# Kernel tuning notes

Measured on AMD Instinct MI355X. Metric: run time of the kernel, lower is better.

## Reference

```python
import jax, jax.numpy as jnp
import numpy as np

N, E, DIM, H = 50000, 800000, 256, 4
HD = DIM // H  # per-head dim = 64
NEG_SLOPE = 0.2
EPS = 1e-5


def _layernorm(x, g, b):
    mu = jnp.mean(x, axis=-1, keepdims=True)
    var = jnp.mean(jnp.square(x - mu), axis=-1, keepdims=True)
    return (x - mu) * jax.lax.rsqrt(var + EPS) * g + b


def setup_inputs() -> dict:
    key = jax.random.key(0)
    ks = jax.random.split(key, 8)
    s = 1.0 / np.sqrt(DIM)
    return {
        "x": jax.random.normal(ks[0], (N, DIM), dtype=jnp.float32),
        "edge_index": jax.random.randint(ks[1], (2, E), 0, N, dtype=jnp.int64),
        "W": jax.random.normal(ks[2], (DIM, DIM), dtype=jnp.float32) * s,
        "a_src": jax.random.normal(ks[3], (H, HD), dtype=jnp.float32) * s,
        "a_dst": jax.random.normal(ks[4], (H, HD), dtype=jnp.float32) * s,
        "gat_b": jnp.zeros((DIM,), jnp.float32),
        "ln1_g": jnp.ones((DIM,), jnp.float32),
        "ln1_b": jnp.zeros((DIM,), jnp.float32),
        "W1": jax.random.normal(ks[5], (DIM, 2 * DIM), dtype=jnp.float32) * s,
        "b1": jnp.zeros((2 * DIM,), jnp.float32),
        "W2": jax.random.normal(ks[6], (2 * DIM, DIM), dtype=jnp.float32) * (1.0 / np.sqrt(2 * DIM)),
        "b2": jnp.zeros((DIM,), jnp.float32),
        "ln2_g": jnp.ones((DIM,), jnp.float32),
        "ln2_b": jnp.zeros((DIM,), jnp.float32),
    }


def _gat(x, edge_index, W, a_src, a_dst, gat_b):
    # add self-loops (PyG GATConv default)
    loops = jnp.arange(N, dtype=edge_index.dtype)
    src = jnp.concatenate([edge_index[0], loops])
    dst = jnp.concatenate([edge_index[1], loops])
    h = (x @ W).reshape(N, H, HD)                    # [N,H,D]
    al_src = jnp.einsum("nhd,hd->nh", h, a_src)      # [N,H]
    al_dst = jnp.einsum("nhd,hd->nh", h, a_dst)
    e = jax.nn.leaky_relu(al_src[src] + al_dst[dst], NEG_SLOPE)  # [E',H]
    # softmax over edges grouped by destination node
    emax = jax.ops.segment_max(e, dst, num_segments=N)           # [N,H]
    ex = jnp.exp(e - emax[dst])
    denom = jax.ops.segment_sum(ex, dst, num_segments=N)         # [N,H]
    alpha = ex / denom[dst]                                      # [E',H]
    msg = alpha[:, :, None] * h[src]                             # [E',H,D]
    out = jax.ops.segment_sum(msg, dst, num_segments=N)          # [N,H,D]
    return out.reshape(N, DIM) + gat_b


def reference(x, edge_index, W, a_src, a_dst, gat_b, ln1_g, ln1_b, W1, b1, W2, b2, ln2_g, ln2_b):
    res = x
    y = _gat(x, edge_index, W, a_src, a_dst, gat_b)
    y = _layernorm(y + res, ln1_g, ln1_b)
    res = y
    f = jax.nn.gelu(y @ W1 + b1, approximate=False) @ W2 + b2
    return _layernorm(f + res, ln2_g, ln2_b)
```

## Files before the change

kernel.cpp:

```cpp
#include <hip/hip_runtime.h>

typedef __bf16 bf16_t;
typedef __bf16 bf16x4 __attribute__((ext_vector_type(4)));
typedef __bf16 bf16x8 __attribute__((ext_vector_type(8)));
typedef float  f32x4  __attribute__((ext_vector_type(4)));
typedef unsigned u32x2 __attribute__((ext_vector_type(2)));

__device__ inline float loadf(const void* p, size_t i, int bf) {
    return bf ? (float)((const bf16_t*)p)[i] : ((const float*)p)[i];
}
__device__ inline int eidx(const void* p, size_t i, int i64) {
    return i64 ? (int)((const long long*)p)[i] : ((const int*)p)[i];
}
__device__ inline float bflo(unsigned u) { return __uint_as_float(u << 16); }
__device__ inline float bfhi(unsigned u) { return __uint_as_float(u & 0xFFFF0000u); }

__device__ inline void gload16(const bf16_t* g, char* l) {
    __builtin_amdgcn_global_load_lds(
        (const __attribute__((address_space(1))) unsigned*)g,
        (__attribute__((address_space(3))) unsigned*)l, 16, 0, 0);
}

__global__ void detect_k(const void* __restrict__ x, const void* __restrict__ ei,
                         int E, int* __restrict__ flags) {
    int l = threadIdx.x;
    const unsigned* xu = (const unsigned*)x;
    unsigned low = xu[l] & 0xFFFFu;
    unsigned ex = (low >> 7) & 0xFF;
    int cnt = __popcll(__ballot(ex >= 115 && ex <= 133));
    const unsigned* eu = (const unsigned*)ei;
    int lim = E < 64 ? E : 64;
    unsigned v = (l < lim) ? eu[2 * (size_t)l + 1] : 0u;
    unsigned long long nz = __ballot(v != 0u);
    if (l == 0) { flags[0] = (cnt >= 32) ? 1 : 0; flags[1] = (nz == 0ull) ? 1 : 0; }
}

__global__ void tobf16_k(const void* __restrict__ in, bf16_t* __restrict__ out,
                         long n, const int* __restrict__ flags) {
    int bf = flags[0];
    long i = ((long)blockIdx.x * 256 + threadIdx.x) * 8;
    long stride = (long)gridDim.x * 256 * 8;
    if (bf) {
        for (; i < n; i += stride)
            *(bf16x8*)&out[i] = *(const bf16x8*)((const bf16_t*)in + i);
    } else {
        for (; i < n; i += stride) {
            f32x4 a = *(const f32x4*)((const float*)in + i);
            f32x4 b = *(const f32x4*)((const float*)in + i + 4);
            bf16x8 r;
            r[0]=(bf16_t)a[0]; r[1]=(bf16_t)a[1]; r[2]=(bf16_t)a[2]; r[3]=(bf16_t)a[3];
            r[4]=(bf16_t)b[0]; r[5]=(bf16_t)b[1]; r[6]=(bf16_t)b[2]; r[7]=(bf16_t)b[3];
            *(bf16x8*)&out[i] = r;
        }
    }
}

__global__ void transpose_k(const void* __restrict__ in, bf16_t* __restrict__ out,
                            int R, int C, const int* __restrict__ flags) {
    int bf = flags[0];
    int i = blockIdx.x * 256 + threadIdx.x;
    if (i < R * C) { int r = i / C, c = i % C; out[c * R + r] = (bf16_t)loadf(in, i, bf); }
}

__global__ __launch_bounds__(256) void gemm128(const bf16_t* __restrict__ A,
                                               const bf16_t* __restrict__ BT,
                                               const void* __restrict__ bias,
                                               bf16_t* __restrict__ C,
                                               int M, int N, int K, int act,
                                               const int* __restrict__ flags,
                                               const void* __restrict__ a_srcp,
                                               const void* __restrict__ a_dstp,
                                               float* __restrict__ alsrc,
                                               float* __restrict__ aldst, int do_al) {
    int bf = flags[0];
    __shared__ __align__(16) char smem[34816];
    int t = threadIdx.x;
    int tm = blockIdx.x * 128;
    int tn = blockIdx.y * 128;
    int w = t >> 6, l = t & 63;
    int wr = (w >> 1) * 64, wc = (w & 1) * 64;
    int lr16 = l & 15, kg = l >> 4;
    int NK = K >> 5;

    f32x4 acc[4][4];
#pragma unroll
    for (int i = 0; i < 4; i++)
#pragma unroll
        for (int j = 0; j < 4; j++) acc[i][j] = (f32x4){0.f, 0.f, 0.f, 0.f};

    bool fast = (tm + 128 <= M);

    if (fast) {
        int buf = 0;
#pragma unroll
        for (int ii = 0; ii < 2; ii++) {
            int c = w + ii * 4;
            int rowa = tm + (c & 1) * 64 + l;
            int rowb = tn + (c & 1) * 64 + l;
            int kc = (c >> 1) * 8;
            gload16(A  + (size_t)rowa * K + kc, smem +         c * 1024 + l * 16);
            gload16(BT + (size_t)rowb * K + kc, smem + 16384 + c * 1024 + l * 16);
        }
        __syncthreads();
        for (int ks = 0; ks < NK; ks++) {
            if (ks + 1 < NK) {
                int k0 = (ks + 1) << 5;
                char* ab = smem + (buf ^ 1) * 8192;
                char* bb = smem + 16384 + (buf ^ 1) * 8192;
#pragma unroll
                for (int ii = 0; ii < 2; ii++) {
                    int c = w + ii * 4;
                    int rowa = tm + (c & 1) * 64 + l;
                    int rowb = tn + (c & 1) * 64 + l;
                    int kc = k0 + (c >> 1) * 8;
                    gload16(A  + (size_t)rowa * K + kc, ab + c * 1024 + l * 16);
                    gload16(BT + (size_t)rowb * K + kc, bb + c * 1024 + l * 16);
                }
            }
            const char* ab = smem + buf * 8192;
            const char* bb = smem + 16384 + buf * 8192;
            bf16x8 af[4], bg[4];
#pragma unroll
            for (int i = 0; i < 4; i++) {
                af[i] = *(const bf16x8*)(ab + ((size_t)(kg * 128 + wr + i * 16 + lr16)) * 16);
                bg[i] = *(const bf16x8*)(bb + ((size_t)(kg * 128 + wc + i * 16 + lr16)) * 16);
            }
#pragma unroll
            for (int i = 0; i < 4; i++)
#pragma unroll
                for (int j = 0; j < 4; j++)
                    acc[i][j] = __builtin_amdgcn_mfma_f32_16x16x32_bf16(af[i], bg[j], acc[i][j], 0, 0, 0);
            __syncthreads();
            buf ^= 1;
        }
    } else {
        int r = t >> 2, kg2 = t & 3;
        for (int ks = 0; ks < NK; ks++) {
            int k0 = ks << 5;
            bf16x8 va[2], vb[2];
#pragma unroll
            for (int j = 0; j < 2; j++) {
                int row = r + j * 64;
                int ra = tm + row; if (ra > M - 1) ra = M - 1;
                va[j] = *(const bf16x8*)(A + (size_t)ra * K + k0 + kg2 * 8);
                vb[j] = *(const bf16x8*)(BT + (size_t)(tn + row) * K + k0 + kg2 * 8);
            }
            __syncthreads();
#pragma unroll
            for (int j = 0; j < 2; j++) {
                int row = r + j * 64;
                *(bf16x8*)(smem + ((size_t)(kg2 * 128 + row)) * 16) = va[j];
                *(bf16x8*)(smem + 16384 + ((size_t)(kg2 * 128 + row)) * 16) = vb[j];
            }
            __syncthreads();
            bf16x8 af[4], bg[4];
#pragma unroll
            for (int i = 0; i < 4; i++) {
                af[i] = *(const bf16x8*)(smem + ((size_t)(kg * 128 + wr + i * 16 + lr16)) * 16);
                bg[i] = *(const bf16x8*)(smem + 16384 + ((size_t)(kg * 128 + wc + i * 16 + lr16)) * 16);
            }
#pragma unroll
            for (int i = 0; i < 4; i++)
#pragma unroll
                for (int j = 0; j < 4; j++)
                    acc[i][j] = __builtin_amdgcn_mfma_f32_16x16x32_bf16(af[i], bg[j], acc[i][j], 0, 0, 0);
        }
        __syncthreads();
    }

    int cr0 = kg * 4;

    if (do_al) {
        float asv[4], adv[4];
#pragma unroll
        for (int j = 0; j < 4; j++) {
            int col = tn + wc + j * 16 + lr16;
            asv[j] = loadf(a_srcp, col, bf);
            adv[j] = loadf(a_dstp, col, bf);
        }
        int head = (tn + wc) >> 6;
#pragma unroll
        for (int i = 0; i < 4; i++) {
#pragma unroll
            for (int q = 0; q < 4; q++) {
                float ps = acc[i][0][q]*asv[0] + acc[i][1][q]*asv[1] + acc[i][2][q]*asv[2] + acc[i][3][q]*asv[3];
                float pd = acc[i][0][q]*adv[0] + acc[i][1][q]*adv[1] + acc[i][2][q]*adv[2] + acc[i][3][q]*adv[3];
#pragma unroll
                for (int d = 1; d < 16; d <<= 1) { ps += __shfl_xor(ps, d); pd += __shfl_xor(pd, d); }
                int row = tm + wr + i * 16 + cr0 + q;
                if (lr16 == 0 && row < M) { alsrc[row * 4 + head] = ps; aldst[row * 4 + head] = pd; }
            }
        }
    }

    bf16_t (*Cst)[136] = (bf16_t(*)[136])smem;
#pragma unroll
    for (int i = 0; i < 4; i++) {
#pragma unroll
        for (int j = 0; j < 4; j++) {
            int col = wc + j * 16 + lr16;
            float bv = bias ? loadf(bias, tn + col, bf) : 0.f;
#pragma unroll
            for (int q = 0; q < 4; q++) {
                float v = acc[i][j][q] + bv;
                if (act) v = 0.5f * v * (1.f + erff(v * 0.70710678118f));
                Cst[wr + i * 16 + cr0 + q][col] = (bf16_t)v;
            }
        }
    }
    __syncthreads();
#pragma unroll
    for (int it = 0; it < 8; it++) {
        int idx = it * 256 + t;
        int row = idx >> 4;
        int c8 = (idx & 15) * 8;
        if (tm + row < M)
            *(bf16x8*)&C[(size_t)(tm + row) * N + tn + c8] = *(const bf16x8*)&Cst[row][c8];
    }
}

__global__ void deg_k(const void* __restrict__ ei, int* __restrict__ deg, int E, int N,
                      const int* __restrict__ flags) {
    int i64 = flags[1];
    int i = blockIdx.x * 256 + threadIdx.x;
    if (i < E) {
        int d = eidx(ei, (size_t)E + i, i64);
        if ((unsigned)d >= (unsigned)N) d = 0;
        atomicAdd(&deg[d], 1);
    }
}

__global__ __launch_bounds__(256) void scan1(const int* __restrict__ deg, int* __restrict__ offs,
                                             int* __restrict__ chunkSum) {
    __shared__ int s[256];
    int t = threadIdx.x, b = blockIdx.x;
    int v = deg[b * 256 + t];
    s[t] = v; __syncthreads();
#pragma unroll
    for (int d = 1; d < 256; d <<= 1) {
        int u = (t >= d) ? s[t - d] : 0;
        __syncthreads(); s[t] += u; __syncthreads();
    }
    offs[b * 256 + t] = s[t] - v;
    if (t == 255) chunkSum[b] = s[255];
}

__global__ __launch_bounds__(256) void scan2(const int* __restrict__ chunkSum, int* __restrict__ chunkOff, int nch) {
    __shared__ int s[256];
    int t = threadIdx.x;
    int v = (t < nch) ? chunkSum[t] : 0;
    s[t] = v; __syncthreads();
#pragma unroll
    for (int d = 1; d < 256; d <<= 1) {
        int u = (t >= d) ? s[t - d] : 0;
        __syncthreads(); s[t] += u; __syncthreads();
    }
    chunkOff[t] = s[t] - v;
}

__global__ void scan3(int* __restrict__ offs, const int* __restrict__ chunkOff,
                      int* __restrict__ cursor, int total) {
    int i = blockIdx.x * 256 + threadIdx.x;
    if (i < total) { int v = offs[i] + chunkOff[i >> 8]; offs[i] = v; cursor[i] = v; }
}

__global__ void scatter_k(const void* __restrict__ ei, int* __restrict__ cursor,
                          int* __restrict__ csr, bf16_t* __restrict__ ewsb,
                          const float* __restrict__ alsrc, const float* __restrict__ aldst,
                          int E, int N, const int* __restrict__ flags) {
    int i64 = flags[1];
    int i = blockIdx.x * 256 + threadIdx.x;
    if (i < E) {
        int s = eidx(ei, i, i64);
        int d = eidx(ei, (size_t)E + i, i64);
        if ((unsigned)s >= (unsigned)N) s = 0;
        if ((unsigned)d >= (unsigned)N) d = 0;
        int p = atomicAdd(&cursor[d], 1);
        csr[p] = s;
        f32x4 as4 = *(const f32x4*)&alsrc[s * 4];
        f32x4 ad4 = *(const f32x4*)&aldst[d * 4];
        bf16x4 w4;
#pragma unroll
        for (int hh = 0; hh < 4; hh++) {
            float e = as4[hh] + ad4[hh];
            e = e > 0.f ? e : 0.2f * e;
            w4[hh] = (bf16_t)expf(fminf(e, 30.f));
        }
        *(bf16x4*)&ewsb[4 * (size_t)p] = w4;
    }
}

__global__ __launch_bounds__(256) void gat_agg_ln(
    const bf16_t* __restrict__ hbuf, const bf16_t* __restrict__ xb,
    const float* __restrict__ alsrc, const float* __restrict__ aldst,
    const int* __restrict__ offs, const int* __restrict__ csr,
    const bf16_t* __restrict__ ewsb,
    const void* __restrict__ gatb, const void* __restrict__ lng, const void* __restrict__ lnb,
    bf16_t* __restrict__ y, const int* __restrict__ flags, int N) {
    int bf = flags[0];
    int w = threadIdx.x >> 6, l = threadIdx.x & 63;
    int n = blockIdx.x * 4 + w;
    if (n >= N) return;
    int h = l >> 4;
    int col0 = l * 4;

    __shared__ int   srcs[4][64];
    __shared__ float ewt[4][4][68];

    int off = offs[n], deg = offs[n + 1] - off;

    float es = alsrc[n * 4 + h] + aldst[n * 4 + h];
    es = es > 0.f ? es : 0.2f * es;
    float wself = expf(fminf(es, 30.f));

    float a0 = 0.f, a1 = 0.f, a2 = 0.f, a3 = 0.f;
    f32x4 ssum = (f32x4){0.f, 0.f, 0.f, 0.f};

    for (int c0 = 0; c0 < deg; c0 += 64) {
        int cl = deg - c0; if (cl > 64) cl = 64;
        if (l < cl) {
            int sv = csr[off + c0 + l];
            srcs[w][l] = sv;
            bf16x4 wv4 = *(const bf16x4*)&ewsb[4 * (size_t)(off + c0 + l)];
            float w0 = (float)wv4[0], w1 = (float)wv4[1], w2 = (float)wv4[2], w3 = (float)wv4[3];
            ewt[w][0][l] = w0; ewt[w][1][l] = w1;
            ewt[w][2][l] = w2; ewt[w][3][l] = w3;
            ssum += (f32x4){w0, w1, w2, w3};
        }
        int i = 0;
        for (; i + 8 <= cl; i += 8) {
            int sv[8]; u32x2 vv[8];
#pragma unroll
            for (int k = 0; k < 8; k++) sv[k] = __builtin_amdgcn_readfirstlane(srcs[w][i + k]);
#pragma unroll
            for (int k = 0; k < 8; k++) vv[k] = ((const u32x2*)(hbuf + (size_t)sv[k] * 256))[l];
            f32x4 wqa = *(const f32x4*)&ewt[w][h][i];
            f32x4 wqb = *(const f32x4*)&ewt[w][h][i + 4];
#pragma unroll
            for (int k = 0; k < 4; k++) {
                a0 += wqa[k]*bflo(vv[k][0]); a1 += wqa[k]*bfhi(vv[k][0]);
                a2 += wqa[k]*bflo(vv[k][1]); a3 += wqa[k]*bfhi(vv[k][1]);
                a0 += wqb[k]*bflo(vv[k+4][0]); a1 += wqb[k]*bfhi(vv[k+4][0]);
                a2 += wqb[k]*bflo(vv[k+4][1]); a3 += wqb[k]*bfhi(vv[k+4][1]);
            }
        }
        for (; i + 4 <= cl; i += 4) {
            int s0 = __builtin_amdgcn_readfirstlane(srcs[w][i]);
            int s1 = __builtin_amdgcn_readfirstlane(srcs[w][i + 1]);
            int s2 = __builtin_amdgcn_readfirstlane(srcs[w][i + 2]);
            int s3 = __builtin_amdgcn_readfirstlane(srcs[w][i + 3]);
            u32x2 v0 = ((const u32x2*)(hbuf + (size_t)s0 * 256))[l];
            u32x2 v1 = ((const u32x2*)(hbuf + (size_t)s1 * 256))[l];
            u32x2 v2 = ((const u32x2*)(hbuf + (size_t)s2 * 256))[l];
            u32x2 v3 = ((const u32x2*)(hbuf + (size_t)s3 * 256))[l];
            f32x4 wq = *(const f32x4*)&ewt[w][h][i];
            a0 += wq[0]*bflo(v0[0]); a1 += wq[0]*bfhi(v0[0]); a2 += wq[0]*bflo(v0[1]); a3 += wq[0]*bfhi(v0[1]);
            a0 += wq[1]*bflo(v1[0]); a1 += wq[1]*bfhi(v1[0]); a2 += wq[1]*bflo(v1[1]); a3 += wq[1]*bfhi(v1[1]);
            a0 += wq[2]*bflo(v2[0]); a1 += wq[2]*bfhi(v2[0]); a2 += wq[2]*bflo(v2[1]); a3 += wq[2]*bfhi(v2[1]);
            a0 += wq[3]*bflo(v3[0]); a1 += wq[3]*bfhi(v3[0]); a2 += wq[3]*bflo(v3[1]); a3 += wq[3]*bfhi(v3[1]);
        }
        for (; i < cl; i++) {
            int sv = __builtin_amdgcn_readfirstlane(srcs[w][i]);
            float wgt = ewt[w][h][i];
            u32x2 v0 = ((const u32x2*)(hbuf + (size_t)sv * 256))[l];
            a0 += wgt*bflo(v0[0]); a1 += wgt*bfhi(v0[0]); a2 += wgt*bflo(v0[1]); a3 += wgt*bfhi(v0[1]);
        }
    }

#pragma unroll
    for (int d = 1; d < 64; d <<= 1) {
        ssum[0] += __shfl_xor(ssum[0], d);
        ssum[1] += __shfl_xor(ssum[1], d);
        ssum[2] += __shfl_xor(ssum[2], d);
        ssum[3] += __shfl_xor(ssum[3], d);
    }
    float dsum = (h == 0) ? ssum[0] : (h == 1) ? ssum[1] : (h == 2) ? ssum[2] : ssum[3];
    float di = 1.f / (dsum + wself);

    u32x2 sv2 = ((const u32x2*)(hbuf + (size_t)n * 256))[l];
    u32x2 xv  = ((const u32x2*)(xb   + (size_t)n * 256))[l];
    float v0f = (a0 + wself*bflo(sv2[0])) * di + loadf(gatb, col0 + 0, bf) + bflo(xv[0]);
    float v1f = (a1 + wself*bfhi(sv2[0])) * di + loadf(gatb, col0 + 1, bf) + bfhi(xv[0]);
    float v2f = (a2 + wself*bflo(sv2[1])) * di + loadf(gatb, col0 + 2, bf) + bflo(xv[1]);
    float v3f = (a3 + wself*bfhi(sv2[1])) * di + loadf(gatb, col0 + 3, bf) + bfhi(xv[1]);

    float s1 = v0f + v1f + v2f + v3f;
#pragma unroll
    for (int d = 1; d < 64; d <<= 1) s1 += __shfl_xor(s1, d);
    float mu = s1 * (1.f / 256.f);
    float c0f = v0f - mu, c1f = v1f - mu, c2f = v2f - mu, c3f = v3f - mu;
    float sq = c0f*c0f + c1f*c1f + c2f*c2f + c3f*c3f;
#pragma unroll
    for (int d = 1; d < 64; d <<= 1) sq += __shfl_xor(sq, d);
    float rs = rsqrtf(sq * (1.f / 256.f) + 1e-5f);

    bf16x4 o;
    o[0] = (bf16_t)(c0f * rs * loadf(lng, col0 + 0, bf) + loadf(lnb, col0 + 0, bf));
    o[1] = (bf16_t)(c1f * rs * loadf(lng, col0 + 1, bf) + loadf(lnb, col0 + 1, bf));
    o[2] = (bf16_t)(c2f * rs * loadf(lng, col0 + 2, bf) + loadf(lnb, col0 + 2, bf));
    o[3] = (bf16_t)(c3f * rs * loadf(lng, col0 + 3, bf) + loadf(lnb, col0 + 3, bf));
    *(bf16x4*)&y[(size_t)n * 256 + col0] = o;
}

__global__ __launch_bounds__(256) void ln_res(const bf16_t* __restrict__ f, const bf16_t* __restrict__ y,
                                              const void* __restrict__ g, const void* __restrict__ b,
                                              void* __restrict__ out, int N, const int* __restrict__ flags) {
    int bf = flags[0];
    int row = blockIdx.x * 4 + (threadIdx.x >> 6);
    int l = threadIdx.x & 63;
    if (row >= N) return;
    int col0 = l * 4;
    u32x2 fv = *(const u32x2*)(f + (size_t)row * 256 + col0);
    u32x2 yv = *(const u32x2*)(y + (size_t)row * 256 + col0);
    float v0 = bflo(fv[0]) + bflo(yv[0]);
    float v1 = bfhi(fv[0]) + bfhi(yv[0]);
    float v2 = bflo(fv[1]) + bflo(yv[1]);
    float v3 = bfhi(fv[1]) + bfhi(yv[1]);
    float s = v0 + v1 + v2 + v3;
#pragma unroll
    for (int d = 1; d < 64; d <<= 1) s += __shfl_xor(s, d);
    float mu = s * (1.f / 256.f);
    float c0 = v0 - mu, c1 = v1 - mu, c2 = v2 - mu, c3 = v3 - mu;
    float sq = c0*c0 + c1*c1 + c2*c2 + c3*c3;
#pragma unroll
    for (int d = 1; d < 64; d <<= 1) sq += __shfl_xor(sq, d);
    float rs = rsqrtf(sq * (1.f / 256.f) + 1e-5f);
    float o0 = c0 * rs * loadf(g, col0 + 0, bf) + loadf(b, col0 + 0, bf);
    float o1 = c1 * rs * loadf(g, col0 + 1, bf) + loadf(b, col0 + 1, bf);
    float o2 = c2 * rs * loadf(g, col0 + 2, bf) + loadf(b, col0 + 2, bf);
    float o3 = c3 * rs * loadf(g, col0 + 3, bf) + loadf(b, col0 + 3, bf);
    if (bf) {
        bf16x4 o; o[0]=(bf16_t)o0; o[1]=(bf16_t)o1; o[2]=(bf16_t)o2; o[3]=(bf16_t)o3;
        *(bf16x4*)&((bf16_t*)out)[(size_t)row * 256 + col0] = o;
    } else {
        f32x4 o = (f32x4){o0, o1, o2, o3};
        *(f32x4*)&((float*)out)[(size_t)row * 256 + col0] = o;
    }
}

extern "C" void kernel_launch(void* const* d_in, const int* in_sizes, int n_in,
                              void* d_out, int out_size, void* d_ws, size_t ws_size,
                              hipStream_t stream) {
    const void* x    = d_in[0];
    const void* ei   = d_in[1];
    const void* W    = d_in[2];
    const void* a_src= d_in[3];
    const void* a_dst= d_in[4];
    const void* gatb = d_in[5];
    const void* ln1g = d_in[6];
    const void* ln1b = d_in[7];
    const void* W1   = d_in[8];
    const void* b1   = d_in[9];
    const void* W2   = d_in[10];
    const void* b2   = d_in[11];
    const void* ln2g = d_in[12];
    const void* ln2b = d_in[13];

    const int DIM = 256, DFF = 512;
    int N = in_sizes[0] / DIM;
    int E = in_sizes[1] / 2;

    char* ws = (char*)d_ws;
    size_t o = 0;
    auto alloc = [&](size_t bytes) { void* p = ws + o; o += (bytes + 255) & ~(size_t)255; return p; };
    int*    flags  = (int*)alloc(256);
    bf16_t* WT     = (bf16_t*)alloc((size_t)DIM * DIM * 2);
    bf16_t* W1T    = (bf16_t*)alloc((size_t)DIM * DFF * 2);
    bf16_t* W2T    = (bf16_t*)alloc((size_t)DFF * DIM * 2);
    float*  alsrc  = (float*)alloc((size_t)N * 4 * 4);
    float*  aldst  = (float*)alloc((size_t)N * 4 * 4);
    int nch = (N + 255) / 256;
    int tot = nch * 256;
    int* deg      = (int*)alloc((size_t)tot * 4);
    int* offs     = (int*)alloc((size_t)(tot + 1) * 4);
    int* cursor   = (int*)alloc((size_t)tot * 4);
    int* chunkSum = (int*)alloc(256 * 4);
    int* chunkOff = (int*)alloc(256 * 4);
    int* csr      = (int*)alloc((size_t)E * 4);
    bf16_t* ewsb  = (bf16_t*)alloc((size_t)E * 8);
    bf16_t* h     = (bf16_t*)alloc((size_t)N * DIM * 2);
    bf16_t* yb    = (bf16_t*)alloc((size_t)N * DIM * 2);
    bf16_t* xb    = (bf16_t*)alloc((size_t)N * DIM * 2);
    bf16_t* fb    = h;
    size_t remain = (ws_size > o) ? (ws_size - o) : 0;
    long CH = (long)(remain / ((size_t)DFF * 2));
    if (CH > N) CH = N;
    if (CH < 1024) CH = 1024;
    bf16_t* t1 = (bf16_t*)alloc((size_t)CH * DFF * 2);

    detect_k<<<1, 64, 0, stream>>>(x, ei, E, flags);
    hipMemsetAsync(deg, 0, (size_t)tot * 4, stream);

    tobf16_k<<<4096, 256, 0, stream>>>(x, xb, (long)N * DIM, flags);
    transpose_k<<<(DIM * DIM + 255) / 256, 256, 0, stream>>>(W,  WT,  DIM, DIM, flags);
    transpose_k<<<(DIM * DFF + 255) / 256, 256, 0, stream>>>(W1, W1T, DIM, DFF, flags);
    transpose_k<<<(DFF * DIM + 255) / 256, 256, 0, stream>>>(W2, W2T, DFF, DIM, flags);

    dim3 g1((N + 127) / 128, DIM / 128);
    gemm128<<<g1, 256, 0, stream>>>(xb, WT, nullptr, h, N, DIM, DIM, 0, flags,
                                    a_src, a_dst, alsrc, aldst, 1);

    deg_k<<<(E + 255) / 256, 256, 0, stream>>>(ei, deg, E, N, flags);
    scan1<<<nch, 256, 0, stream>>>(deg, offs, chunkSum);
    scan2<<<1, 256, 0, stream>>>(chunkSum, chunkOff, nch);
    scan3<<<(tot + 255) / 256, 256, 0, stream>>>(offs, chunkOff, cursor, tot);
    scatter_k<<<(E + 255) / 256, 256, 0, stream>>>(ei, cursor, csr, ewsb, alsrc, aldst, E, N, flags);

    gat_agg_ln<<<(N + 3) / 4, 256, 0, stream>>>(h, xb, alsrc, aldst, offs, csr, ewsb,
                                                gatb, ln1g, ln1b, yb, flags, N);

    for (long r0 = 0; r0 < N; r0 += CH) {
        int m = (int)((N - r0 < CH) ? (N - r0) : CH);
        dim3 g2((m + 127) / 128, DFF / 128);
        gemm128<<<g2, 256, 0, stream>>>(yb + r0 * DIM, W1T, b1, t1, m, DFF, DIM, 1, flags,
                                        nullptr, nullptr, nullptr, nullptr, 0);
        dim3 g3((m + 127) / 128, DIM / 128);
        gemm128<<<g3, 256, 0, stream>>>(t1, W2T, b2, fb + r0 * DIM, m, DIM, DFF, 0, flags,
                                        nullptr, nullptr, nullptr, nullptr, 0);
    }

    ln_res<<<(N + 3) / 4, 256, 0, stream>>>(fb, yb, ln2g, ln2b, d_out, N, flags);
}
```

Before: 367.0 us.

## Add 128x256-tile GEMM kernel for the FFN matmuls

Adds a new gemm_wide kernel with 128x256 output tiles: each wave computes a 64x128 sub-tile, and the kernel uses double-buffered global_load_lds staging. The two FFN GEMMs (W1 with GELU and W2) now use it instead of gemm128. Wider tiles are meant to raise operand reuse per LDS load and halve the number of blocks along N. In exchange, each thread holds far more accumulators, which can lower occupancy, and the epilogue is staged in two halves.

Measured after the change: 563.9 us. 53.7% more time.

```diff
diff --git a/kernel.cpp b/kernel.cpp
--- a/kernel.cpp
+++ b/kernel.cpp
@@ -216,6 +216,149 @@
         int c8 = (idx & 15) * 8;
         if (tm + row < M)
             *(bf16x8*)&C[(size_t)(tm + row) * N + tn + c8] = *(const bf16x8*)&Cst[row][c8];
+    }
+}
+
+__global__ __launch_bounds__(256) void gemm_wide(const bf16_t* __restrict__ A,
+                                                 const bf16_t* __restrict__ BT,
+                                                 const void* __restrict__ bias,
+                                                 bf16_t* __restrict__ C,
+                                                 int M, int N, int K, int act,
+                                                 const int* __restrict__ flags) {
+    int bf = flags[0];
+    __shared__ __align__(16) char smem[49152];
+    int t = threadIdx.x;
+    int tm = blockIdx.x * 128;
+    int tn = blockIdx.y * 256;
+    int w = t >> 6, l = t & 63;
+    int wr = (w >> 1) * 64, wc = (w & 1) * 128;
+    int lr16 = l & 15, kg = l >> 4;
+    int NK = K >> 5;
+
+    f32x4 acc[4][8];
+#pragma unroll
+    for (int i = 0; i < 4; i++)
+#pragma unroll
+        for (int j = 0; j < 8; j++) acc[i][j] = (f32x4){0.f, 0.f, 0.f, 0.f};
+
+    bool fast = (tm + 128 <= M);
+
+    if (fast) {
+        int buf = 0;
+#pragma unroll
+        for (int ii = 0; ii < 2; ii++) {
+            int c = w + ii * 4;
+            int rowa = tm + (c & 1) * 64 + l;
+            gload16(A + (size_t)rowa * K + (c >> 1) * 8, smem + c * 1024 + l * 16);
+        }
+#pragma unroll
+        for (int ii = 0; ii < 4; ii++) {
+            int rowb = tn + w * 64 + l;
+            gload16(BT + (size_t)rowb * K + ii * 8, smem + 16384 + (w + ii * 4) * 1024 + l * 16);
+        }
+        __syncthreads();
+        for (int ks = 0; ks < NK; ks++) {
+            if (ks + 1 < NK) {
+                int k0 = (ks + 1) << 5;
+                char* ab = smem + (buf ^ 1) * 8192;
+                char* bb = smem + 16384 + (buf ^ 1) * 16384;
+#pragma unroll
+                for (int ii = 0; ii < 2; ii++) {
+                    int c = w + ii * 4;
+                    int rowa = tm + (c & 1) * 64 + l;
+                    gload16(A + (size_t)rowa * K + k0 + (c >> 1) * 8, ab + c * 1024 + l * 16);
+                }
+#pragma unroll
+                for (int ii = 0; ii < 4; ii++) {
+                    int rowb = tn + w * 64 + l;
+                    gload16(BT + (size_t)rowb * K + k0 + ii * 8, bb + (w + ii * 4) * 1024 + l * 16);
+                }
+            }
+            const char* ab = smem + buf * 8192;
+            const char* bb = smem + 16384 + buf * 16384;
+            bf16x8 af[4], bg[8];
+#pragma unroll
+            for (int i = 0; i < 4; i++)
+                af[i] = *(const bf16x8*)(ab + (size_t)(kg * 2048 + (wr + i * 16 + lr16) * 16));
+#pragma unroll
+            for (int j = 0; j < 8; j++)
+                bg[j] = *(const bf16x8*)(bb + (size_t)(kg * 4096 + (wc + j * 16 + lr16) * 16));
+#pragma unroll
+            for (int i = 0; i < 4; i++)
+#pragma unroll
+                for (int j = 0; j < 8; j++)
+                    acc[i][j] = __builtin_amdgcn_mfma_f32_16x16x32_bf16(af[i], bg[j], acc[i][j], 0, 0, 0);
+            __syncthreads();
+            buf ^= 1;
+        }
+    } else {
+        for (int ks = 0; ks < NK; ks++) {
+            int k0 = ks << 5;
+            bf16x8 va[2], vb[4];
+#pragma unroll
+            for (int ii = 0; ii < 2; ii++) {
+                int c = w + ii * 4;
+                int ra = tm + (c & 1) * 64 + l; if (ra > M - 1) ra = M - 1;
+                va[ii] = *(const bf16x8*)(A + (size_t)ra * K + k0 + (c >> 1) * 8);
+            }
+#pragma unroll
+            for (int ii = 0; ii < 4; ii++)
+                vb[ii] = *(const bf16x8*)(BT + (size_t)(tn + w * 64 + l) * K + k0 + ii * 8);
+            __syncthreads();
+#pragma unroll
+            for (int ii = 0; ii < 2; ii++)
+                *(bf16x8*)(smem + (w + ii * 4) * 1024 + l * 16) = va[ii];
+#pragma unroll
+            for (int ii = 0; ii < 4; ii++)
+                *(bf16x8*)(smem + 16384 + (w + ii * 4) * 1024 + l * 16) = vb[ii];
+            __syncthreads();
+            bf16x8 af[4], bg[8];
+#pragma unroll
+            for (int i = 0; i < 4; i++)
+                af[i] = *(const bf16x8*)(smem + (size_t)(kg * 2048 + (wr + i * 16 + lr16) * 16));
+#pragma unroll
+            for (int j = 0; j < 8; j++)
+                bg[j] = *(const bf16x8*)(smem + 16384 + (size_t)(kg * 4096 + (wc + j * 16 + lr16) * 16));
+#pragma unroll
+            for (int i = 0; i < 4; i++)
+#pragma unroll
+                for (int j = 0; j < 8; j++)
+                    acc[i][j] = __builtin_amdgcn_mfma_f32_16x16x32_bf16(af[i], bg[j], acc[i][j], 0, 0, 0);
+        }
+        __syncthreads();
+    }
+
+    bf16_t (*Cst)[264] = (bf16_t(*)[264])smem;
+    int cr0 = kg * 4;
+#pragma unroll
+    for (int half = 0; half < 2; half++) {
+        if ((w >> 1) == half) {
+#pragma unroll
+            for (int i = 0; i < 4; i++) {
+#pragma unroll
+                for (int j = 0; j < 8; j++) {
+                    int col = wc + j * 16 + lr16;
+                    float bv = bias ? loadf(bias, tn + col, bf) : 0.f;
+#pragma unroll
+                    for (int q = 0; q < 4; q++) {
+                        float v = acc[i][j][q] + bv;
+                        if (act) v = 0.5f * v * (1.f + erff(v * 0.70710678118f));
+                        Cst[i * 16 + cr0 + q][col] = (bf16_t)v;
+                    }
+                }
+            }
+        }
+        __syncthreads();
+#pragma unroll
+        for (int it = 0; it < 8; it++) {
+            int idx = it * 256 + t;
+            int row = idx >> 5;
+            int c8 = (idx & 31) * 8;
+            int gr = tm + half * 64 + row;
+            if (gr < M)
+                *(bf16x8*)&C[(size_t)gr * N + tn + c8] = *(const bf16x8*)&Cst[row][c8];
+        }
+        __syncthreads();
     }
 }
 
@@ -511,12 +654,10 @@
 
     for (long r0 = 0; r0 < N; r0 += CH) {
         int m = (int)((N - r0 < CH) ? (N - r0) : CH);
-        dim3 g2((m + 127) / 128, DFF / 128);
-        gemm128<<<g2, 256, 0, stream>>>(yb + r0 * DIM, W1T, b1, t1, m, DFF, DIM, 1, flags,
-                                        nullptr, nullptr, nullptr, nullptr, 0);
-        dim3 g3((m + 127) / 128, DIM / 128);
-        gemm128<<<g3, 256, 0, stream>>>(t1, W2T, b2, fb + r0 * DIM, m, DIM, DFF, 0, flags,
-                                        nullptr, nullptr, nullptr, nullptr, 0);
+        dim3 g2((m + 127) / 128, DFF / 256);
+        gemm_wide<<<g2, 256, 0, stream>>>(yb + r0 * DIM, W1T, b1, t1, m, DFF, DIM, 1, flags);
+        dim3 g3((m + 127) / 128, DIM / 256);
+        gemm_wide<<<g3, 256, 0, stream>>>(t1, W2T, b2, fb + r0 * DIM, m, DIM, DFF, 0, flags);
     }
 
     ln_res<<<(N + 3) / 4, 256, 0, stream>>>(fb, yb, ln2g, ln2b, d_out, N, flags);
```
